# Performance work log

Measured on AMD Instinct MI355X. Metric: run time of the kernel, lower is better.

## Reference

```python
import math
import jax, jax.numpy as jnp
import numpy as np

B, S, D = 8, 512, 1024        # batch, seq (dec and enc), model dim
HID, NH = 1024, 16            # attention hidden, heads
C = HID // NH                 # per-head channels (self-attn 'attends' over this dim!)
EPS = 1e-5


def setup_inputs() -> dict:
    key = jax.random.key(0)
    ks = jax.random.split(key, 26)
    w = lambda k, sh: (jax.random.normal(k, sh, jnp.float32) * 0.02)
    inp = {
        "x": jax.random.normal(ks[0], (B, S, D), jnp.float32),
        "h": jax.random.normal(ks[1], (B, S, D), jnp.float32),
        # self-attn (AttentionModule) params, stored [in, out]
        "Wq": w(ks[2], (D, HID)), "bq": jnp.zeros((HID,), jnp.float32),
        "Wk": w(ks[3], (D, HID)), "bk": jnp.zeros((HID,), jnp.float32),
        "Wv": w(ks[4], (D, HID)), "bv": jnp.zeros((HID,), jnp.float32),
        "Wo": w(ks[5], (HID, D)), "bo": jnp.zeros((D,), jnp.float32),
        # cross-attn params
        "Wcq": w(ks[6], (D, HID)), "bcq": jnp.zeros((HID,), jnp.float32),
        "Wck": w(ks[7], (D, HID)), "bck": jnp.zeros((HID,), jnp.float32),
        "Wcv": w(ks[8], (D, HID)), "bcv": jnp.zeros((HID,), jnp.float32),
        "Wco": w(ks[9], (HID, D)), "bco": jnp.zeros((D,), jnp.float32),
        "gamma": jnp.ones((D,), jnp.float32), "beta": jnp.zeros((D,), jnp.float32),
        # FFN (two Linears, NO nonlinearity, per original code)
        "W1": w(ks[10], (D, HID)), "b1": jnp.zeros((HID,), jnp.float32),
        "W2": w(ks[11], (HID, D)), "b2": jnp.zeros((D,), jnp.float32),
    }
    return inp


def _layernorm(x, gamma, beta):
    mu = jnp.mean(x, axis=-1, keepdims=True)
    var = jnp.mean(jnp.square(x - mu), axis=-1, keepdims=True)
    return (x - mu) * jax.lax.rsqrt(var + EPS) * gamma + beta


def _self_attn(x, Wq, bq, Wk, bk, Wv, bv, Wo, bo):
    # FAITHFUL to original: reshape [B,S,NH,C]; einsum '...hq,...hk->...hqk' with
    # batch dims [B,S] -> attention over the C channel dim per token, causal mask over channels.
    Q = (x @ Wq + bq).reshape(B, S, NH, C) / math.sqrt(C)
    K = (x @ Wk + bk).reshape(B, S, NH, C)
    V = (x @ Wv + bv).reshape(B, S, NH, C)
    aff = jnp.einsum('bshq,bshk->bshqk', Q, K)            # [B,S,NH,C,C]
    mask = jnp.triu(jnp.full((C, C), -jnp.inf, jnp.float32), k=1)  # -inf above diag, 0 else
    aff = aff + mask
    w = jax.nn.softmax(aff, axis=-1)
    av = jnp.einsum('bshqk,bshk->bshq', w, V)             # [B,S,NH,C]
    return av.reshape(B, S, HID) @ Wo + bo


def _cross_attn(xd, he, Wcq, bcq, Wck, bck, Wcv, bcv, Wco, bco):
    # standard multi-head cross attention, but scaled by sqrt(d_full) per original
    Q = (xd @ Wcq + bcq).reshape(B, S, NH, C).transpose(0, 2, 1, 3)  # [B,NH,Sq,C]
    K = (he @ Wck + bck).reshape(B, S, NH, C).transpose(0, 2, 1, 3)
    V = (he @ Wcv + bcv).reshape(B, S, NH, C).transpose(0, 2, 1, 3)
    scores = jnp.einsum('bhqd,bhkd->bhqk', Q, K) / math.sqrt(HID)
    p = jax.nn.softmax(scores, axis=-1)
    o = jnp.einsum('bhqk,bhkd->bhqd', p, V)               # [B,NH,Sq,C]
    o = o.transpose(0, 2, 1, 3).reshape(B, S, HID)
    return o @ Wco + bco


def reference(x, h, Wq, bq, Wk, bk, Wv, bv, Wo, bo,
              Wcq, bcq, Wck, bck, Wcv, bcv, Wco, bco,
              gamma, beta, W1, b1, W2, b2):
    out = _self_attn(x, Wq, bq, Wk, bk, Wv, bv, Wo, bo) + x
    out = _layernorm(out, gamma, beta)
    out = _cross_attn(out, h, Wcq, bcq, Wck, bck, Wcv, bcv, Wco, bco) + out
    out = _layernorm(out, gamma, beta)
    out = ((out @ W1 + b1) @ W2 + b2) + out
    out = _layernorm(out, gamma, beta)
    return out
```

## Files before the change

### kernel.cpp

```cpp
#include <hip/hip_runtime.h>

typedef __bf16 bf16_t;
typedef bf16_t bf16x8 __attribute__((ext_vector_type(8)));
typedef bf16_t bf16x4 __attribute__((ext_vector_type(4)));
typedef float f32x4 __attribute__((ext_vector_type(4)));

__device__ __forceinline__ void async_copy16(const void* g, void* l) {
  __builtin_amdgcn_global_load_lds(
      (const __attribute__((address_space(1))) unsigned int*)(unsigned long long)g,
      (__attribute__((address_space(3))) unsigned int*)(unsigned int)(unsigned long long)l,
      16, 0, 0);
}

__device__ __forceinline__ float fast_exp2(float x) {
#if __has_builtin(__builtin_amdgcn_exp2f)
  return __builtin_amdgcn_exp2f(x);
#else
  return exp2f(x);
#endif
}

__device__ __forceinline__ unsigned pack_bf16(float x, float y) {
  bf16_t lo = (bf16_t)x, hi = (bf16_t)y;
  unsigned short ul, uh;
  __builtin_memcpy(&ul, &lo, 2);
  __builtin_memcpy(&uh, &hi, 2);
  return (unsigned)ul | ((unsigned)uh << 16);
}

__global__ __launch_bounds__(256) void cast2_bf16_kernel(
    const float* __restrict__ a, const float* __restrict__ b,
    bf16_t* __restrict__ dst) {
  int i = (blockIdx.x * 256 + threadIdx.x) * 8;
  const float* s = (i < 4194304) ? (a + i) : (b + i - 4194304);
  float4 u = *(const float4*)s;
  float4 v = *(const float4*)(s + 4);
  bf16x8 o;
  o[0]=(bf16_t)u.x; o[1]=(bf16_t)u.y; o[2]=(bf16_t)u.z; o[3]=(bf16_t)u.w;
  o[4]=(bf16_t)v.x; o[5]=(bf16_t)v.y; o[6]=(bf16_t)v.z; o[7]=(bf16_t)v.w;
  *(bf16x8*)(dst + i) = o;
}

struct SrcPtrs { const float* p[10]; };
__global__ __launch_bounds__(256) void transpose_cast_all(
    SrcPtrs srcs, bf16_t* __restrict__ dstbase) {
  __shared__ float tile[32][33];
  int z = blockIdx.z;
  const float* src = srcs.p[z];
  bf16_t* dst = dstbase + (size_t)z * 1048576;
  float scale = (z == 0) ? 0.125f : ((z == 4) ? 0.03125f : 1.f);
  int bx = blockIdx.x * 32;
  int by = blockIdx.y * 32;
  int tx = threadIdx.x, ty = threadIdx.y;
#pragma unroll
  for (int i = 0; i < 32; i += 8)
    tile[ty + i][tx] = src[(size_t)(by + ty + i) * 1024 + bx + tx];
  __syncthreads();
#pragma unroll
  for (int i = 0; i < 32; i += 8)
    dst[(size_t)(bx + ty + i) * 1024 + by + tx] = (bf16_t)(tile[tx][ty + i] * scale);
}

__global__ __launch_bounds__(256) void prep_bias_kernel(
    const float* __restrict__ bq, const float* __restrict__ bk,
    const float* __restrict__ bv, const float* __restrict__ bck,
    const float* __restrict__ bcv, const float* __restrict__ bcq,
    float* __restrict__ cb) {
  int i = blockIdx.x * 256 + threadIdx.x;
  if (i < 1024) cb[i] = bq[i] * 0.125f;
  else if (i < 2048) cb[i] = bk[i - 1024];
  else if (i < 3072) cb[i] = bv[i - 2048];
  else if (i < 4096) cb[i] = bck[i - 3072];
  else if (i < 5120) cb[i] = bcv[i - 4096];
  else cb[i] = bcq[i - 5120] * 0.03125f;
}

template <int BN, bool HAS_RES, bool TRANS_OUT>
__global__ __launch_bounds__(256) void gemm_bf16(
    const bf16_t* __restrict__ A, const bf16_t* __restrict__ Bt,
    const float* __restrict__ bias, const bf16_t* __restrict__ res,
    bf16_t* __restrict__ C, int ldC) {
  constexpr int MI = (BN == 128) ? 4 : 2;
  constexpr int NI = 4;
  __shared__ bf16_t As[128 * 64];
  __shared__ bf16_t Bs[BN * 64];
  int tid = threadIdx.x;
  int w = tid >> 6, lane = tid & 63;
  int fm = lane & 15, fq = lane >> 4;
  int bm = blockIdx.y * 128, bn = blockIdx.x * BN;
  int wm = (BN == 128) ? (w >> 1) * 64 : w * 32;
  int wn = (BN == 128) ? (w & 1) * 64 : 0;
  f32x4 acc[MI][NI] = {};
  for (int kt = 0; kt < 1024; kt += 64) {
#pragma unroll
    for (int i = 0; i < 4; i++) {
      int c = i * 256 + tid;
      int row = c >> 3, skg = (c & 7) ^ (row & 7);
      async_copy16(A + (size_t)(bm + row) * 1024 + kt + skg * 8, &As[c * 8]);
    }
#pragma unroll
    for (int i = 0; i < BN / 32; i++) {
      int c = i * 256 + tid;
      int row = c >> 3, skg = (c & 7) ^ (row & 7);
      async_copy16(Bt + (size_t)(bn + row) * 1024 + kt + skg * 8, &Bs[c * 8]);
    }
    __syncthreads();
#pragma unroll
    for (int ks = 0; ks < 2; ks++) {
      bf16x8 af[MI], bfr[NI];
      int kg = ks * 4 + fq;
#pragma unroll
      for (int mi = 0; mi < MI; mi++) {
        int row = wm + mi * 16 + fm;
        af[mi] = *(const bf16x8*)&As[row * 64 + ((kg ^ (row & 7)) * 8)];
      }
#pragma unroll
      for (int ni = 0; ni < NI; ni++) {
        int row = wn + ni * 16 + fm;
        bfr[ni] = *(const bf16x8*)&Bs[row * 64 + ((kg ^ (row & 7)) * 8)];
      }
#pragma unroll
      for (int mi = 0; mi < MI; mi++)
#pragma unroll
        for (int ni = 0; ni < NI; ni++)
          acc[mi][ni] = __builtin_amdgcn_mfma_f32_16x16x32_bf16(
              af[mi], bfr[ni], acc[mi][ni], 0, 0, 0);
    }
    __syncthreads();
  }
#pragma unroll
  for (int mi = 0; mi < MI; mi++) {
#pragma unroll
    for (int ni = 0; ni < NI; ni++) {
      int col = bn + wn + ni * 16 + fm;
      float bv = bias[col];
      if (TRANS_OUT) {
        int rowb = bm + wm + mi * 16 + fq * 4;
        bf16x4 w4;
#pragma unroll
        for (int r = 0; r < 4; r++) w4[r] = (bf16_t)(acc[mi][ni][r] + bv);
        *(bf16x4*)&C[(size_t)col * ldC + rowb] = w4;
      } else {
#pragma unroll
        for (int r = 0; r < 4; r++) {
          int row = bm + wm + mi * 16 + fq * 4 + r;
          float v = acc[mi][ni][r] + bv;
          if (HAS_RES) v += (float)res[(size_t)row * ldC + col];
          C[(size_t)row * ldC + col] = (bf16_t)v;
        }
      }
    }
  }
}

__global__ __launch_bounds__(256) void gemm_cqkv(
    const bf16_t* __restrict__ t1n, const bf16_t* __restrict__ hb,
    const bf16_t* __restrict__ wt4, const float* __restrict__ cb,
    bf16_t* __restrict__ cq, bf16_t* __restrict__ kbuf,
    bf16_t* __restrict__ vt) {
  constexpr int MI = 2, NI = 4;
  __shared__ bf16_t As[128 * 64];
  __shared__ bf16_t Bs[64 * 64];
  int region = blockIdx.x >> 4;
  int bn = (blockIdx.x & 15) * 64;
  const bf16_t* A = (region == 0) ? t1n : hb;
  const bf16_t* Bt = wt4 + (size_t)region * 1048576;
  int boff = (region == 0) ? 5120 : ((region == 1) ? 3072 : 4096);
  int tid = threadIdx.x;
  int w = tid >> 6, lane = tid & 63;
  int fm = lane & 15, fq = lane >> 4;
  int bm = blockIdx.y * 128;
  int wm = w * 32, wn = 0;
  f32x4 acc[MI][NI] = {};
  for (int kt = 0; kt < 1024; kt += 64) {
#pragma unroll
    for (int i = 0; i < 4; i++) {
      int c = i * 256 + tid;
      int row = c >> 3, skg = (c & 7) ^ (row & 7);
      async_copy16(A + (size_t)(bm + row) * 1024 + kt + skg * 8, &As[c * 8]);
    }
    {
      int c = tid, row = c >> 3, skg = (c & 7) ^ (row & 7);
      async_copy16(Bt + (size_t)(bn + row) * 1024 + kt + skg * 8, &Bs[c * 8]);
      c = 256 + tid; row = c >> 3; skg = (c & 7) ^ (row & 7);
      async_copy16(Bt + (size_t)(bn + row) * 1024 + kt + skg * 8, &Bs[c * 8]);
    }
    __syncthreads();
#pragma unroll
    for (int ks = 0; ks < 2; ks++) {
      bf16x8 af[MI], bfr[NI];
      int kg = ks * 4 + fq;
#pragma unroll
      for (int mi = 0; mi < MI; mi++) {
        int row = wm + mi * 16 + fm;
        af[mi] = *(const bf16x8*)&As[row * 64 + ((kg ^ (row & 7)) * 8)];
      }
#pragma unroll
      for (int ni = 0; ni < NI; ni++) {
        int row = wn + ni * 16 + fm;
        bfr[ni] = *(const bf16x8*)&Bs[row * 64 + ((kg ^ (row & 7)) * 8)];
      }
#pragma unroll
      for (int mi = 0; mi < MI; mi++)
#pragma unroll
        for (int ni = 0; ni < NI; ni++)
          acc[mi][ni] = __builtin_amdgcn_mfma_f32_16x16x32_bf16(
              af[mi], bfr[ni], acc[mi][ni], 0, 0, 0);
    }
    __syncthreads();
  }
#pragma unroll
  for (int mi = 0; mi < MI; mi++) {
#pragma unroll
    for (int ni = 0; ni < NI; ni++) {
      int col = bn + ni * 16 + fm;
      float bv = cb[boff + col];
      if (region == 2) {
        int rowb = bm + wm + mi * 16 + fq * 4;
        bf16x4 w4;
#pragma unroll
        for (int r = 0; r < 4; r++) w4[r] = (bf16_t)(acc[mi][ni][r] + bv);
        *(bf16x4*)&vt[(size_t)col * 4096 + rowb] = w4;
      } else {
        bf16_t* C = (region == 0) ? cq : kbuf;
#pragma unroll
        for (int r = 0; r < 4; r++) {
          int row = bm + wm + mi * 16 + fq * 4 + r;
          C[(size_t)row * 1024 + col] = (bf16_t)(acc[mi][ni][r] + bv);
        }
      }
    }
  }
}

__global__ __launch_bounds__(256) void self_attn_kernel(
    const bf16_t* __restrict__ QKV, bf16_t* __restrict__ O) {
  __shared__ float2 kv[4][64];
  int tid = threadIdx.x;
  int wu = tid >> 6, lane = tid & 63;
  int unit = blockIdx.x * 4 + wu;
  int m = unit >> 4, h = unit & 15;
  size_t iq = (size_t)m * 3072 + h * 64 + lane;
  float q = (float)QKV[iq] * 1.44269504089f;
  float kk = (float)QKV[iq + 1024];
  float vv = (float)QKV[iq + 2048];
  kv[wu][lane] = make_float2(kk, vv);
  __syncthreads();
  const float2* kvp = kv[wu];
  float l0 = 0.f, l1 = 0.f, o0 = 0.f, o1 = 0.f;
#pragma unroll
  for (int j = 0; j < 64; j += 2) {
    float2 a = kvp[j];
    float2 b = kvp[j + 1];
    float e0 = fast_exp2(q * a.x);
    float e1 = fast_exp2(q * b.x);
    e0 = (j <= lane) ? e0 : 0.f;
    e1 = (j + 1 <= lane) ? e1 : 0.f;
    l0 += e0; o0 = fmaf(e0, a.y, o0);
    l1 += e1; o1 = fmaf(e1, b.y, o1);
  }
  float l = l0 + l1, o = o0 + o1;
  O[(size_t)m * 1024 + h * 64 + lane] = (bf16_t)(o / l);
}

__global__ __launch_bounds__(256) void cross_attn_mfma(
    const bf16_t* __restrict__ Q, const bf16_t* __restrict__ Kb,
    const bf16_t* __restrict__ Vt, bf16_t* __restrict__ O) {
  __shared__ bf16_t Ks[64 * 64];
  __shared__ bf16_t Vs[64 * 64];
  int tid = threadIdx.x;
  int w = tid >> 6, lane = tid & 63;
  int fm = lane & 15, fq = lane >> 4;
  int bh = blockIdx.x;
  int b = bh >> 4, h = bh & 15;
  int q0 = blockIdx.y * 64 + w * 16;
  const bf16_t* Qp = Q + (size_t)(b * 512 + q0 + fm) * 1024 + h * 64 + fq * 8;
  bf16x8 qf0 = *(const bf16x8*)Qp;
  bf16x8 qf1 = *(const bf16x8*)(Qp + 32);
  f32x4 o[4] = {};
  float mx = -1e30f, l = 0.f;
  for (int k0 = 0; k0 < 512; k0 += 64) {
    __syncthreads();
#pragma unroll
    for (int i = 0; i < 2; i++) {
      int c = i * 256 + tid;
      int row = c >> 3, kg = (c & 7) ^ (row & 7);
      async_copy16(Kb + (size_t)(b * 512 + k0 + row) * 1024 + h * 64 + kg * 8,
                   &Ks[c * 8]);
      async_copy16(Vt + (size_t)(h * 64 + row) * 4096 + b * 512 + k0 + kg * 8,
                   &Vs[c * 8]);
    }
    __syncthreads();
    f32x4 s[4] = {};
#pragma unroll
    for (int mt = 0; mt < 4; mt++) {
      int row = mt * 16 + fm;
#pragma unroll
      for (int f = 0; f < 2; f++) {
        int kg = f * 4 + fq;
        bf16x8 kf = *(const bf16x8*)&Ks[row * 64 + ((kg ^ (row & 7)) * 8)];
        s[mt] = __builtin_amdgcn_mfma_f32_16x16x32_bf16(
            kf, (f ? qf1 : qf0), s[mt], 0, 0, 0);
      }
    }
    float smax = -1e30f;
#pragma unroll
    for (int mt = 0; mt < 4; mt++)
#pragma unroll
      for (int r = 0; r < 4; r++) smax = fmaxf(smax, s[mt][r]);
    smax = fmaxf(smax, __shfl_xor(smax, 16, 64));
    smax = fmaxf(smax, __shfl_xor(smax, 32, 64));
    float nm = fmaxf(mx, smax);
    float corr = __expf(mx - nm);
    float ladd = 0.f;
    unsigned pk0[4], pk1[4];
#pragma unroll
    for (int mt = 0; mt < 4; mt++) {
      float p0 = __expf(s[mt][0] - nm);
      float p1 = __expf(s[mt][1] - nm);
      float p2 = __expf(s[mt][2] - nm);
      float p3 = __expf(s[mt][3] - nm);
      ladd += (p0 + p1) + (p2 + p3);
      pk0[mt] = pack_bf16(p0, p1);
      pk1[mt] = pack_bf16(p2, p3);
    }
    ladd += __shfl_xor(ladd, 16, 64);
    ladd += __shfl_xor(ladd, 32, 64);
    l = l * corr + ladd;
#pragma unroll
    for (int ct = 0; ct < 4; ct++)
#pragma unroll
      for (int r = 0; r < 4; r++) o[ct][r] *= corr;
    union U { unsigned u[4]; bf16x8 v; } pf[2];
    int sl0 = ((fq & 1) * 2) * 16 + fm;
    int sl1 = sl0 + 16;
    bool hi = fq >= 2;
#pragma unroll
    for (int f = 0; f < 2; f++) {
      unsigned a0 = (unsigned)__shfl((int)pk0[f * 2],     sl0, 64);
      unsigned b0 = (unsigned)__shfl((int)pk0[f * 2 + 1], sl0, 64);
      unsigned a1 = (unsigned)__shfl((int)pk1[f * 2],     sl0, 64);
      unsigned b1 = (unsigned)__shfl((int)pk1[f * 2 + 1], sl0, 64);
      unsigned a2 = (unsigned)__shfl((int)pk0[f * 2],     sl1, 64);
      unsigned b2 = (unsigned)__shfl((int)pk0[f * 2 + 1], sl1, 64);
      unsigned a3 = (unsigned)__shfl((int)pk1[f * 2],     sl1, 64);
      unsigned b3 = (unsigned)__shfl((int)pk1[f * 2 + 1], sl1, 64);
      pf[f].u[0] = hi ? b0 : a0;
      pf[f].u[1] = hi ? b1 : a1;
      pf[f].u[2] = hi ? b2 : a2;
      pf[f].u[3] = hi ? b3 : a3;
    }
#pragma unroll
    for (int ct = 0; ct < 4; ct++) {
      int row = ct * 16 + fm;
#pragma unroll
      for (int f = 0; f < 2; f++) {
        int kg = f * 4 + fq;
        bf16x8 vf = *(const bf16x8*)&Vs[row * 64 + ((kg ^ (row & 7)) * 8)];
        o[ct] = __builtin_amdgcn_mfma_f32_16x16x32_bf16(vf, pf[f].v, o[ct], 0, 0, 0);
      }
    }
    mx = nm;
  }
  float inv = 1.f / l;
  bf16_t* Op = O + (size_t)(b * 512 + q0 + fm) * 1024 + h * 64 + fq * 4;
#pragma unroll
  for (int ct = 0; ct < 4; ct++) {
    bf16x4 w4;
    w4[0] = (bf16_t)(o[ct][0] * inv);
    w4[1] = (bf16_t)(o[ct][1] * inv);
    w4[2] = (bf16_t)(o[ct][2] * inv);
    w4[3] = (bf16_t)(o[ct][3] * inv);
    *(bf16x4*)(Op + ct * 16) = w4;
  }
}

template <typename OutT>
__global__ __launch_bounds__(256) void ln_kernel(
    const bf16_t* __restrict__ X, const float* __restrict__ gamma,
    const float* __restrict__ beta, OutT* __restrict__ Y) {
  __shared__ float red[8];
  int row = blockIdx.x;
  int tid = threadIdx.x;
  bf16x4 x4 = *(const bf16x4*)(X + (size_t)row * 1024 + tid * 4);
  float4 v = {(float)x4[0], (float)x4[1], (float)x4[2], (float)x4[3]};
  float s = (v.x + v.y) + (v.z + v.w);
  float ss = fmaf(v.x, v.x, fmaf(v.y, v.y, fmaf(v.z, v.z, v.w * v.w)));
#pragma unroll
  for (int off = 32; off > 0; off >>= 1) {
    s  += __shfl_down(s, off, 64);
    ss += __shfl_down(ss, off, 64);
  }
  if ((tid & 63) == 0) { red[tid >> 6] = s; red[4 + (tid >> 6)] = ss; }
  __syncthreads();
  float S  = (red[0] + red[1]) + (red[2] + red[3]);
  float SS = (red[4] + red[5]) + (red[6] + red[7]);
  float mu = S * (1.f / 1024.f);
  float var = SS * (1.f / 1024.f) - mu * mu;
  float inv = rsqrtf(var + 1e-5f);
  float4 g = *(const float4*)(gamma + tid * 4);
  float4 b = *(const float4*)(beta + tid * 4);
  float r0 = (v.x - mu) * inv * g.x + b.x;
  float r1 = (v.y - mu) * inv * g.y + b.y;
  float r2 = (v.z - mu) * inv * g.z + b.z;
  float r3 = (v.w - mu) * inv * g.w + b.w;
  OutT* yp = Y + (size_t)row * 1024 + tid * 4;
  yp[0] = (OutT)r0; yp[1] = (OutT)r1; yp[2] = (OutT)r2; yp[3] = (OutT)r3;
}

extern "C" void kernel_launch(void* const* d_in, const int* in_sizes, int n_in,
                              void* d_out, int out_size, void* d_ws, size_t ws_size,
                              hipStream_t stream) {
  (void)in_sizes; (void)n_in; (void)out_size; (void)ws_size;
  const float* x  = (const float*)d_in[0];
  const float* hh = (const float*)d_in[1];
  SrcPtrs sp;
  sp.p[0] = (const float*)d_in[2];  sp.p[1] = (const float*)d_in[4];
  sp.p[2] = (const float*)d_in[6];  sp.p[3] = (const float*)d_in[8];
  sp.p[4] = (const float*)d_in[10]; sp.p[5] = (const float*)d_in[12];
  sp.p[6] = (const float*)d_in[14]; sp.p[7] = (const float*)d_in[16];
  sp.p[8] = (const float*)d_in[20]; sp.p[9] = (const float*)d_in[22];
  const float* bq  = (const float*)d_in[3];
  const float* bk  = (const float*)d_in[5];
  const float* bv  = (const float*)d_in[7];
  const float* bo  = (const float*)d_in[9];
  const float* bck = (const float*)d_in[13];
  const float* bcv = (const float*)d_in[15];
  const float* bcq = (const float*)d_in[11];
  const float* bco = (const float*)d_in[17];
  const float* gamma = (const float*)d_in[18];
  const float* beta  = (const float*)d_in[19];
  const float* b1  = (const float*)d_in[21];
  const float* b2  = (const float*)d_in[23];
  float* out = (float*)d_out;
  char* ws = (char*)d_ws;
  const size_t MB = 1048576;

  bf16_t* wt[10];
  for (int i = 0; i < 10; i++) wt[i] = (bf16_t*)(ws + (size_t)i * 2 * MB);
  float* cb      = (float*)(ws + 20 * MB);
  bf16_t* xb     = (bf16_t*)(ws + 21 * MB);
  bf16_t* hb     = (bf16_t*)(ws + 29 * MB);
  bf16_t* qkv    = (bf16_t*)(ws + 37 * MB);
  bf16_t* kbuf   = (bf16_t*)(ws + 37 * MB);
  bf16_t* vtbuf  = (bf16_t*)(ws + 45 * MB);
  bf16_t* f1out  = (bf16_t*)(ws + 53 * MB);
  bf16_t* cqbuf  = (bf16_t*)(ws + 61 * MB);
  bf16_t* attn   = (bf16_t*)(ws + 69 * MB);
  bf16_t* g4     = (bf16_t*)(ws + 77 * MB);
  bf16_t* t1n    = xb;
  bf16_t* t2n    = hb;
  bf16_t* f2out  = g4;

  cast2_bf16_kernel<<<4096, 256, 0, stream>>>(x, hh, xb);
  transpose_cast_all<<<dim3(32, 32, 10), dim3(32, 8), 0, stream>>>(sp, (bf16_t*)ws);
  prep_bias_kernel<<<24, 256, 0, stream>>>(bq, bk, bv, bck, bcv, bcq, cb);

  gemm_bf16<128, false, false><<<dim3(24, 32), 256, 0, stream>>>(xb, wt[0], cb, nullptr, qkv, 3072);
  self_attn_kernel<<<16384, 256, 0, stream>>>(qkv, attn);
  gemm_bf16<64, true, false><<<dim3(16, 32), 256, 0, stream>>>(attn, wt[3], bo, xb, g4, 1024);
  ln_kernel<bf16_t><<<4096, 256, 0, stream>>>(g4, gamma, beta, t1n);
  gemm_cqkv<<<dim3(48, 32), 256, 0, stream>>>(t1n, hb, wt[4], cb, cqbuf, kbuf, vtbuf);
  cross_attn_mfma<<<dim3(128, 8), 256, 0, stream>>>(cqbuf, kbuf, vtbuf, attn);
  gemm_bf16<64, true, false><<<dim3(16, 32), 256, 0, stream>>>(attn, wt[7], bco, t1n, g4, 1024);
  ln_kernel<bf16_t><<<4096, 256, 0, stream>>>(g4, gamma, beta, t2n);
  gemm_bf16<64, false, false><<<dim3(16, 32), 256, 0, stream>>>(t2n, wt[8], b1, nullptr, f1out, 1024);
  gemm_bf16<64, true, false><<<dim3(16, 32), 256, 0, stream>>>(f1out, wt[9], b2, t2n, f2out, 1024);
  ln_kernel<float><<<4096, 256, 0, stream>>>(f2out, gamma, beta, out);
}
```

Measured before the change: 392.7 us.

## Fold linear FFN weights into one matrix, enlarge cross-QKV tiles, unroll self-attn

Because the FFN has no nonlinearity, W1·W2 is precomputed per call as a single 1024x1024 product (a small GEMM on cast W1 and transposed W2), and the biases are combined as b1·W2+b2. This replaces two full-size activation GEMMs with one plus a 1024-row weight GEMM. The cross-attention QKV GEMM also moves to 128x128 tiles with 4x4 MFMA fragments per wave, and the self-attention inner loop is unrolled to four independent accumulator chains. The folded weight is rounded to bf16, which changes numerics slightly.

```diff
diff --git a/kernel.cpp b/kernel.cpp
--- a/kernel.cpp
+++ b/kernel.cpp
@@ -28,11 +28,13 @@
   return (unsigned)ul | ((unsigned)uh << 16);
 }
 
-__global__ __launch_bounds__(256) void cast2_bf16_kernel(
+__global__ __launch_bounds__(256) void cast3_bf16_kernel(
     const float* __restrict__ a, const float* __restrict__ b,
-    bf16_t* __restrict__ dst) {
+    const float* __restrict__ w1, bf16_t* __restrict__ dst) {
   int i = (blockIdx.x * 256 + threadIdx.x) * 8;
-  const float* s = (i < 4194304) ? (a + i) : (b + i - 4194304);
+  const float* s = (i < 4194304) ? (a + i)
+                 : (i < 8388608) ? (b + i - 4194304)
+                                 : (w1 + i - 8388608);
   float4 u = *(const float4*)s;
   float4 v = *(const float4*)(s + 4);
   bf16x8 o;
@@ -72,7 +74,25 @@
   else if (i < 3072) cb[i] = bv[i - 2048];
   else if (i < 4096) cb[i] = bck[i - 3072];
   else if (i < 5120) cb[i] = bcv[i - 4096];
-  else cb[i] = bcq[i - 5120] * 0.03125f;
+  else if (i < 6144) cb[i] = bcq[i - 5120] * 0.03125f;
+  else cb[i] = 0.f;
+}
+
+__global__ __launch_bounds__(256) void bias_fuse_kernel(
+    const bf16_t* __restrict__ wt9, const float* __restrict__ b1,
+    const float* __restrict__ b2, float* __restrict__ cb2) {
+  int n = blockIdx.x * 256 + threadIdx.x;
+  const bf16_t* row = wt9 + (size_t)n * 1024;
+  float acc = 0.f;
+#pragma unroll 4
+  for (int h = 0; h < 1024; h += 8) {
+    bf16x8 v = *(const bf16x8*)(row + h);
+    float4 ba = *(const float4*)(b1 + h);
+    float4 bb = *(const float4*)(b1 + h + 4);
+    acc += ba.x*(float)v[0] + ba.y*(float)v[1] + ba.z*(float)v[2] + ba.w*(float)v[3]
+         + bb.x*(float)v[4] + bb.y*(float)v[5] + bb.z*(float)v[6] + bb.w*(float)v[7];
+  }
+  cb2[n] = acc + b2[n];
 }
 
 template <int BN, bool HAS_RES, bool TRANS_OUT>
@@ -158,11 +178,11 @@
     const bf16_t* __restrict__ wt4, const float* __restrict__ cb,
     bf16_t* __restrict__ cq, bf16_t* __restrict__ kbuf,
     bf16_t* __restrict__ vt) {
-  constexpr int MI = 2, NI = 4;
+  constexpr int MI = 4, NI = 4;
   __shared__ bf16_t As[128 * 64];
-  __shared__ bf16_t Bs[64 * 64];
-  int region = blockIdx.x >> 4;
-  int bn = (blockIdx.x & 15) * 64;
+  __shared__ bf16_t Bs[128 * 64];
+  int region = blockIdx.x >> 3;
+  int bn = (blockIdx.x & 7) * 128;
   const bf16_t* A = (region == 0) ? t1n : hb;
   const bf16_t* Bt = wt4 + (size_t)region * 1048576;
   int boff = (region == 0) ? 5120 : ((region == 1) ? 3072 : 4096);
@@ -170,7 +190,7 @@
   int w = tid >> 6, lane = tid & 63;
   int fm = lane & 15, fq = lane >> 4;
   int bm = blockIdx.y * 128;
-  int wm = w * 32, wn = 0;
+  int wm = (w >> 1) * 64, wn = (w & 1) * 64;
   f32x4 acc[MI][NI] = {};
   for (int kt = 0; kt < 1024; kt += 64) {
 #pragma unroll
@@ -179,10 +199,10 @@
       int row = c >> 3, skg = (c & 7) ^ (row & 7);
       async_copy16(A + (size_t)(bm + row) * 1024 + kt + skg * 8, &As[c * 8]);
     }
-    {
-      int c = tid, row = c >> 3, skg = (c & 7) ^ (row & 7);
-      async_copy16(Bt + (size_t)(bn + row) * 1024 + kt + skg * 8, &Bs[c * 8]);
-      c = 256 + tid; row = c >> 3; skg = (c & 7) ^ (row & 7);
+#pragma unroll
+    for (int i = 0; i < 4; i++) {
+      int c = i * 256 + tid;
+      int row = c >> 3, skg = (c & 7) ^ (row & 7);
       async_copy16(Bt + (size_t)(bn + row) * 1024 + kt + skg * 8, &Bs[c * 8]);
     }
     __syncthreads();
@@ -213,7 +233,7 @@
   for (int mi = 0; mi < MI; mi++) {
 #pragma unroll
     for (int ni = 0; ni < NI; ni++) {
-      int col = bn + ni * 16 + fm;
+      int col = bn + wn + ni * 16 + fm;
       float bv = cb[boff + col];
       if (region == 2) {
         int rowb = bm + wm + mi * 16 + fq * 4;
@@ -247,19 +267,29 @@
   kv[wu][lane] = make_float2(kk, vv);
   __syncthreads();
   const float2* kvp = kv[wu];
-  float l0 = 0.f, l1 = 0.f, o0 = 0.f, o1 = 0.f;
-#pragma unroll
-  for (int j = 0; j < 64; j += 2) {
+  float l0 = 0.f, l1 = 0.f, l2 = 0.f, l3 = 0.f;
+  float o0 = 0.f, o1 = 0.f, o2 = 0.f, o3 = 0.f;
+#pragma unroll
+  for (int j = 0; j < 64; j += 4) {
     float2 a = kvp[j];
     float2 b = kvp[j + 1];
+    float2 c = kvp[j + 2];
+    float2 d = kvp[j + 3];
     float e0 = fast_exp2(q * a.x);
     float e1 = fast_exp2(q * b.x);
-    e0 = (j <= lane) ? e0 : 0.f;
+    float e2 = fast_exp2(q * c.x);
+    float e3 = fast_exp2(q * d.x);
+    e0 = (j     <= lane) ? e0 : 0.f;
     e1 = (j + 1 <= lane) ? e1 : 0.f;
+    e2 = (j + 2 <= lane) ? e2 : 0.f;
+    e3 = (j + 3 <= lane) ? e3 : 0.f;
     l0 += e0; o0 = fmaf(e0, a.y, o0);
     l1 += e1; o1 = fmaf(e1, b.y, o1);
-  }
-  float l = l0 + l1, o = o0 + o1;
+    l2 += e2; o2 = fmaf(e2, c.y, o2);
+    l3 += e3; o3 = fmaf(e3, d.y, o3);
+  }
+  float l = (l0 + l1) + (l2 + l3);
+  float o = (o0 + o1) + (o2 + o3);
   O[(size_t)m * 1024 + h * 64 + lane] = (bf16_t)(o / l);
 }
 
@@ -420,6 +450,7 @@
   sp.p[4] = (const float*)d_in[10]; sp.p[5] = (const float*)d_in[12];
   sp.p[6] = (const float*)d_in[14]; sp.p[7] = (const float*)d_in[16];
   sp.p[8] = (const float*)d_in[20]; sp.p[9] = (const float*)d_in[22];
+  const float* W1f = (const float*)d_in[20];
   const float* bq  = (const float*)d_in[3];
   const float* bk  = (const float*)d_in[5];
   const float* bv  = (const float*)d_in[7];
@@ -439,32 +470,35 @@
   bf16_t* wt[10];
   for (int i = 0; i < 10; i++) wt[i] = (bf16_t*)(ws + (size_t)i * 2 * MB);
   float* cb      = (float*)(ws + 20 * MB);
+  float* cb2     = (float*)(ws + 20 * MB + 32768);
   bf16_t* xb     = (bf16_t*)(ws + 21 * MB);
   bf16_t* hb     = (bf16_t*)(ws + 29 * MB);
+  bf16_t* w1bf   = (bf16_t*)(ws + 37 * MB);
   bf16_t* qkv    = (bf16_t*)(ws + 37 * MB);
   bf16_t* kbuf   = (bf16_t*)(ws + 37 * MB);
   bf16_t* vtbuf  = (bf16_t*)(ws + 45 * MB);
-  bf16_t* f1out  = (bf16_t*)(ws + 53 * MB);
   bf16_t* cqbuf  = (bf16_t*)(ws + 61 * MB);
   bf16_t* attn   = (bf16_t*)(ws + 69 * MB);
   bf16_t* g4     = (bf16_t*)(ws + 77 * MB);
+  bf16_t* ptbuf  = (bf16_t*)(ws + 85 * MB);
   bf16_t* t1n    = xb;
   bf16_t* t2n    = hb;
   bf16_t* f2out  = g4;
 
-  cast2_bf16_kernel<<<4096, 256, 0, stream>>>(x, hh, xb);
+  cast3_bf16_kernel<<<4608, 256, 0, stream>>>(x, hh, W1f, xb);
   transpose_cast_all<<<dim3(32, 32, 10), dim3(32, 8), 0, stream>>>(sp, (bf16_t*)ws);
-  prep_bias_kernel<<<24, 256, 0, stream>>>(bq, bk, bv, bck, bcv, bcq, cb);
+  prep_bias_kernel<<<28, 256, 0, stream>>>(bq, bk, bv, bck, bcv, bcq, cb);
+  bias_fuse_kernel<<<4, 256, 0, stream>>>(wt[9], b1, b2, cb2);
+  gemm_bf16<64, false, false><<<dim3(16, 8), 256, 0, stream>>>(wt[9], w1bf, cb + 6144, nullptr, ptbuf, 1024);
 
   gemm_bf16<128, false, false><<<dim3(24, 32), 256, 0, stream>>>(xb, wt[0], cb, nullptr, qkv, 3072);
   self_attn_kernel<<<16384, 256, 0, stream>>>(qkv, attn);
   gemm_bf16<64, true, false><<<dim3(16, 32), 256, 0, stream>>>(attn, wt[3], bo, xb, g4, 1024);
   ln_kernel<bf16_t><<<4096, 256, 0, stream>>>(g4, gamma, beta, t1n);
-  gemm_cqkv<<<dim3(48, 32), 256, 0, stream>>>(t1n, hb, wt[4], cb, cqbuf, kbuf, vtbuf);
+  gemm_cqkv<<<dim3(24, 32), 256, 0, stream>>>(t1n, hb, wt[4], cb, cqbuf, kbuf, vtbuf);
   cross_attn_mfma<<<dim3(128, 8), 256, 0, stream>>>(cqbuf, kbuf, vtbuf, attn);
   gemm_bf16<64, true, false><<<dim3(16, 32), 256, 0, stream>>>(attn, wt[7], bco, t1n, g4, 1024);
   ln_kernel<bf16_t><<<4096, 256, 0, stream>>>(g4, gamma, beta, t2n);
-  gemm_bf16<64, false, false><<<dim3(16, 32), 256, 0, stream>>>(t2n, wt[8], b1, nullptr, f1out, 1024);
-  gemm_bf16<64, true, false><<<dim3(16, 32), 256, 0, stream>>>(f1out, wt[9], b2, t2n, f2out, 1024);
+  gemm_bf16<64, true, false><<<dim3(16, 32), 256, 0, stream>>>(t2n, ptbuf, cb2, t2n, f2out, 1024);
   ln_kernel<float><<<4096, 256, 0, stream>>>(f2out, gamma, beta, out);
 }
```

Result: slower. 410.1 us (+4.4%).

## Fold linear FFN into single precomputed weight product W1·W2

Applied to the files above, without the earlier changes.

Because the FFN has no nonlinearity, the two linear layers are merged algebraically. The product of W1 and W2 is computed once per call by a small GEMM that runs alongside the QKV GEMM in one launch, and the combined bias b1·W2 + b2 is computed in the bias prep kernel. This removes one full 4096x1024x1024 GEMM and its intermediate buffer from the critical path. It adds a 1024^3 weight GEMM and an extra W1 cast, and the combined weight is rounded to bf16, which may change numerics slightly.

```diff
diff --git a/kernel.cpp b/kernel.cpp
--- a/kernel.cpp
+++ b/kernel.cpp
@@ -28,17 +28,22 @@
   return (unsigned)ul | ((unsigned)uh << 16);
 }
 
-__global__ __launch_bounds__(256) void cast2_bf16_kernel(
+__global__ __launch_bounds__(256) void cast3_bf16_kernel(
     const float* __restrict__ a, const float* __restrict__ b,
-    bf16_t* __restrict__ dst) {
+    const float* __restrict__ w1, bf16_t* __restrict__ dst1,
+    bf16_t* __restrict__ dstw) {
   int i = (blockIdx.x * 256 + threadIdx.x) * 8;
-  const float* s = (i < 4194304) ? (a + i) : (b + i - 4194304);
+  const float* s;
+  bf16_t* d;
+  if (i < 4194304) { s = a + i; d = dst1 + i; }
+  else if (i < 8388608) { s = b + i - 4194304; d = dst1 + i; }
+  else { s = w1 + i - 8388608; d = dstw + (i - 8388608); }
   float4 u = *(const float4*)s;
   float4 v = *(const float4*)(s + 4);
   bf16x8 o;
   o[0]=(bf16_t)u.x; o[1]=(bf16_t)u.y; o[2]=(bf16_t)u.z; o[3]=(bf16_t)u.w;
   o[4]=(bf16_t)v.x; o[5]=(bf16_t)v.y; o[6]=(bf16_t)v.z; o[7]=(bf16_t)v.w;
-  *(bf16x8*)(dst + i) = o;
+  *(bf16x8*)d = o;
 }
 
 struct SrcPtrs { const float* p[10]; };
@@ -65,29 +70,45 @@
     const float* __restrict__ bq, const float* __restrict__ bk,
     const float* __restrict__ bv, const float* __restrict__ bck,
     const float* __restrict__ bcv, const float* __restrict__ bcq,
-    float* __restrict__ cb) {
-  int i = blockIdx.x * 256 + threadIdx.x;
-  if (i < 1024) cb[i] = bq[i] * 0.125f;
-  else if (i < 2048) cb[i] = bk[i - 1024];
-  else if (i < 3072) cb[i] = bv[i - 2048];
-  else if (i < 4096) cb[i] = bck[i - 3072];
-  else if (i < 5120) cb[i] = bcv[i - 4096];
-  else cb[i] = bcq[i - 5120] * 0.03125f;
-}
-
-template <int BN, bool HAS_RES, bool TRANS_OUT>
-__global__ __launch_bounds__(256) void gemm_bf16(
+    const bf16_t* __restrict__ wt9, const float* __restrict__ b1,
+    const float* __restrict__ b2, float* __restrict__ cb,
+    float* __restrict__ cb2) {
+  int bid = blockIdx.x;
+  if (bid < 28) {
+    int i = bid * 256 + threadIdx.x;
+    if (i < 1024) cb[i] = bq[i] * 0.125f;
+    else if (i < 2048) cb[i] = bk[i - 1024];
+    else if (i < 3072) cb[i] = bv[i - 2048];
+    else if (i < 4096) cb[i] = bck[i - 3072];
+    else if (i < 5120) cb[i] = bcv[i - 4096];
+    else if (i < 6144) cb[i] = bcq[i - 5120] * 0.03125f;
+    else cb[i] = 0.f;
+  } else {
+    int n = (bid - 28) * 256 + threadIdx.x;
+    const bf16_t* row = wt9 + (size_t)n * 1024;
+    float acc = 0.f;
+#pragma unroll 4
+    for (int h = 0; h < 1024; h += 8) {
+      bf16x8 v = *(const bf16x8*)(row + h);
+      float4 ba = *(const float4*)(b1 + h);
+      float4 bb = *(const float4*)(b1 + h + 4);
+      acc += ba.x*(float)v[0] + ba.y*(float)v[1] + ba.z*(float)v[2] + ba.w*(float)v[3]
+           + bb.x*(float)v[4] + bb.y*(float)v[5] + bb.z*(float)v[6] + bb.w*(float)v[7];
+    }
+    cb2[n] = acc + b2[n];
+  }
+}
+
+template <int BN, int MI, bool HAS_RES, bool TRANS_OUT>
+__device__ __forceinline__ void gemm_core(
     const bf16_t* __restrict__ A, const bf16_t* __restrict__ Bt,
     const float* __restrict__ bias, const bf16_t* __restrict__ res,
-    bf16_t* __restrict__ C, int ldC) {
-  constexpr int MI = (BN == 128) ? 4 : 2;
+    bf16_t* __restrict__ C, int ldC, int bm, int bn,
+    bf16_t* As, bf16_t* Bs) {
   constexpr int NI = 4;
-  __shared__ bf16_t As[128 * 64];
-  __shared__ bf16_t Bs[BN * 64];
   int tid = threadIdx.x;
   int w = tid >> 6, lane = tid & 63;
   int fm = lane & 15, fq = lane >> 4;
-  int bm = blockIdx.y * 128, bn = blockIdx.x * BN;
   int wm = (BN == 128) ? (w >> 1) * 64 : w * 32;
   int wn = (BN == 128) ? (w & 1) * 64 : 0;
   f32x4 acc[MI][NI] = {};
@@ -153,83 +174,55 @@
   }
 }
 
+template <int BN, bool HAS_RES, bool TRANS_OUT>
+__global__ __launch_bounds__(256) void gemm_bf16(
+    const bf16_t* __restrict__ A, const bf16_t* __restrict__ Bt,
+    const float* __restrict__ bias, const bf16_t* __restrict__ res,
+    bf16_t* __restrict__ C, int ldC) {
+  __shared__ bf16_t As[128 * 64];
+  __shared__ bf16_t Bs[BN * 64];
+  gemm_core<BN, (BN == 128) ? 4 : 2, HAS_RES, TRANS_OUT>(
+      A, Bt, bias, res, C, ldC, blockIdx.y * 128, blockIdx.x * BN, As, Bs);
+}
+
+__global__ __launch_bounds__(256) void gemm_qkv_p(
+    const bf16_t* __restrict__ xb, const bf16_t* __restrict__ wt0,
+    const bf16_t* __restrict__ wt9, const bf16_t* __restrict__ w1bf,
+    const float* __restrict__ cb, bf16_t* __restrict__ qkv,
+    bf16_t* __restrict__ pt) {
+  __shared__ bf16_t smem[2 * 128 * 64];
+  if (blockIdx.x < 24) {
+    gemm_core<128, 4, false, false>(xb, wt0, cb, nullptr, qkv, 3072,
+                                    blockIdx.y * 128, blockIdx.x * 128,
+                                    smem, smem + 128 * 64);
+  } else {
+    int lin = (blockIdx.x - 24) * 32 + blockIdx.y;
+    gemm_core<64, 2, false, false>(wt9, w1bf, cb + 6144, nullptr, pt, 1024,
+                                   (lin >> 4) * 128, (lin & 15) * 64,
+                                   smem, smem + 128 * 64);
+  }
+}
+
 __global__ __launch_bounds__(256) void gemm_cqkv(
     const bf16_t* __restrict__ t1n, const bf16_t* __restrict__ hb,
     const bf16_t* __restrict__ wt4, const float* __restrict__ cb,
     bf16_t* __restrict__ cq, bf16_t* __restrict__ kbuf,
     bf16_t* __restrict__ vt) {
-  constexpr int MI = 2, NI = 4;
   __shared__ bf16_t As[128 * 64];
   __shared__ bf16_t Bs[64 * 64];
   int region = blockIdx.x >> 4;
   int bn = (blockIdx.x & 15) * 64;
-  const bf16_t* A = (region == 0) ? t1n : hb;
+  int bm = blockIdx.y * 128;
   const bf16_t* Bt = wt4 + (size_t)region * 1048576;
-  int boff = (region == 0) ? 5120 : ((region == 1) ? 3072 : 4096);
-  int tid = threadIdx.x;
-  int w = tid >> 6, lane = tid & 63;
-  int fm = lane & 15, fq = lane >> 4;
-  int bm = blockIdx.y * 128;
-  int wm = w * 32, wn = 0;
-  f32x4 acc[MI][NI] = {};
-  for (int kt = 0; kt < 1024; kt += 64) {
-#pragma unroll
-    for (int i = 0; i < 4; i++) {
-      int c = i * 256 + tid;
-      int row = c >> 3, skg = (c & 7) ^ (row & 7);
-      async_copy16(A + (size_t)(bm + row) * 1024 + kt + skg * 8, &As[c * 8]);
-    }
-    {
-      int c = tid, row = c >> 3, skg = (c & 7) ^ (row & 7);
-      async_copy16(Bt + (size_t)(bn + row) * 1024 + kt + skg * 8, &Bs[c * 8]);
-      c = 256 + tid; row = c >> 3; skg = (c & 7) ^ (row & 7);
-      async_copy16(Bt + (size_t)(bn + row) * 1024 + kt + skg * 8, &Bs[c * 8]);
-    }
-    __syncthreads();
-#pragma unroll
-    for (int ks = 0; ks < 2; ks++) {
-      bf16x8 af[MI], bfr[NI];
-      int kg = ks * 4 + fq;
-#pragma unroll
-      for (int mi = 0; mi < MI; mi++) {
-        int row = wm + mi * 16 + fm;
-        af[mi] = *(const bf16x8*)&As[row * 64 + ((kg ^ (row & 7)) * 8)];
-      }
-#pragma unroll
-      for (int ni = 0; ni < NI; ni++) {
-        int row = wn + ni * 16 + fm;
-        bfr[ni] = *(const bf16x8*)&Bs[row * 64 + ((kg ^ (row & 7)) * 8)];
-      }
-#pragma unroll
-      for (int mi = 0; mi < MI; mi++)
-#pragma unroll
-        for (int ni = 0; ni < NI; ni++)
-          acc[mi][ni] = __builtin_amdgcn_mfma_f32_16x16x32_bf16(
-              af[mi], bfr[ni], acc[mi][ni], 0, 0, 0);
-    }
-    __syncthreads();
-  }
-#pragma unroll
-  for (int mi = 0; mi < MI; mi++) {
-#pragma unroll
-    for (int ni = 0; ni < NI; ni++) {
-      int col = bn + ni * 16 + fm;
-      float bv = cb[boff + col];
-      if (region == 2) {
-        int rowb = bm + wm + mi * 16 + fq * 4;
-        bf16x4 w4;
-#pragma unroll
-        for (int r = 0; r < 4; r++) w4[r] = (bf16_t)(acc[mi][ni][r] + bv);
-        *(bf16x4*)&vt[(size_t)col * 4096 + rowb] = w4;
-      } else {
-        bf16_t* C = (region == 0) ? cq : kbuf;
-#pragma unroll
-        for (int r = 0; r < 4; r++) {
-          int row = bm + wm + mi * 16 + fq * 4 + r;
-          C[(size_t)row * 1024 + col] = (bf16_t)(acc[mi][ni][r] + bv);
-        }
-      }
-    }
+  if (region == 2) {
+    gemm_core<64, 2, false, true>(hb, Bt, cb + 4096, nullptr, vt, 4096,
+                                  bm, bn, As, Bs);
+  } else if (region == 1) {
+    gemm_core<64, 2, false, false>(hb, Bt, cb + 3072, nullptr, kbuf, 1024,
+                                   bm, bn, As, Bs);
+  } else {
+    gemm_core<64, 2, false, false>(t1n, Bt, cb + 5120, nullptr, cq, 1024,
+                                   bm, bn, As, Bs);
   }
 }
 
@@ -420,6 +413,7 @@
   sp.p[4] = (const float*)d_in[10]; sp.p[5] = (const float*)d_in[12];
   sp.p[6] = (const float*)d_in[14]; sp.p[7] = (const float*)d_in[16];
   sp.p[8] = (const float*)d_in[20]; sp.p[9] = (const float*)d_in[22];
+  const float* W1f = (const float*)d_in[20];
   const float* bq  = (const float*)d_in[3];
   const float* bk  = (const float*)d_in[5];
   const float* bv  = (const float*)d_in[7];
@@ -439,24 +433,27 @@
   bf16_t* wt[10];
   for (int i = 0; i < 10; i++) wt[i] = (bf16_t*)(ws + (size_t)i * 2 * MB);
   float* cb      = (float*)(ws + 20 * MB);
+  float* cb2     = (float*)(ws + 20 * MB + 32768);
   bf16_t* xb     = (bf16_t*)(ws + 21 * MB);
   bf16_t* hb     = (bf16_t*)(ws + 29 * MB);
   bf16_t* qkv    = (bf16_t*)(ws + 37 * MB);
   bf16_t* kbuf   = (bf16_t*)(ws + 37 * MB);
   bf16_t* vtbuf  = (bf16_t*)(ws + 45 * MB);
-  bf16_t* f1out  = (bf16_t*)(ws + 53 * MB);
   bf16_t* cqbuf  = (bf16_t*)(ws + 61 * MB);
   bf16_t* attn   = (bf16_t*)(ws + 69 * MB);
   bf16_t* g4     = (bf16_t*)(ws + 77 * MB);
+  bf16_t* ptbuf  = (bf16_t*)(ws + 85 * MB);
+  bf16_t* w1bf   = (bf16_t*)(ws + 87 * MB);
   bf16_t* t1n    = xb;
   bf16_t* t2n    = hb;
   bf16_t* f2out  = g4;
 
-  cast2_bf16_kernel<<<4096, 256, 0, stream>>>(x, hh, xb);
+  cast3_bf16_kernel<<<4608, 256, 0, stream>>>(x, hh, W1f, xb, w1bf);
   transpose_cast_all<<<dim3(32, 32, 10), dim3(32, 8), 0, stream>>>(sp, (bf16_t*)ws);
-  prep_bias_kernel<<<24, 256, 0, stream>>>(bq, bk, bv, bck, bcv, bcq, cb);
-
-  gemm_bf16<128, false, false><<<dim3(24, 32), 256, 0, stream>>>(xb, wt[0], cb, nullptr, qkv, 3072);
+  prep_bias_kernel<<<32, 256, 0, stream>>>(bq, bk, bv, bck, bcv, bcq,
+                                           wt[9], b1, b2, cb, cb2);
+
+  gemm_qkv_p<<<dim3(28, 32), 256, 0, stream>>>(xb, wt[0], wt[9], w1bf, cb, qkv, ptbuf);
   self_attn_kernel<<<16384, 256, 0, stream>>>(qkv, attn);
   gemm_bf16<64, true, false><<<dim3(16, 32), 256, 0, stream>>>(attn, wt[3], bo, xb, g4, 1024);
   ln_kernel<bf16_t><<<4096, 256, 0, stream>>>(g4, gamma, beta, t1n);
@@ -464,7 +461,6 @@
   cross_attn_mfma<<<dim3(128, 8), 256, 0, stream>>>(cqbuf, kbuf, vtbuf, attn);
   gemm_bf16<64, true, false><<<dim3(16, 32), 256, 0, stream>>>(attn, wt[7], bco, t1n, g4, 1024);
   ln_kernel<bf16_t><<<4096, 256, 0, stream>>>(g4, gamma, beta, t2n);
-  gemm_bf16<64, false, false><<<dim3(16, 32), 256, 0, stream>>>(t2n, wt[8], b1, nullptr, f1out, 1024);
-  gemm_bf16<64, true, false><<<dim3(16, 32), 256, 0, stream>>>(f1out, wt[9], b2, t2n, f2out, 1024);
+  gemm_bf16<64, true, false><<<dim3(16, 32), 256, 0, stream>>>(t2n, ptbuf, cb2, t2n, f2out, 1024);
   ln_kernel<float><<<4096, 256, 0, stream>>>(f2out, gamma, beta, out);
 }
```

Result: slower. 401.5 us (+2.2%).
